# Kernel tuning notes

Measured on AMD Instinct MI355X. Metric: run time of the kernel, lower is better.

## Reference

```python
import jax, jax.numpy as jnp
import numpy as np

B, L, F, H = 1024, 256, 128, 256
A, CH, OUT = 128, 256, 512


def setup_inputs() -> dict:
    key = jax.random.key(0)
    ks = jax.random.split(key, 12)
    s = lambda k, shape, fan: (jax.random.normal(k, shape, jnp.float32) / np.float32(np.sqrt(fan)))
    return dict(
        input_batch=jax.random.normal(ks[0], (B, L, F), jnp.float32),
        tte=jax.random.randint(ks[1], (B,), 0, L, jnp.int32),
        W_ih=s(ks[2], (3 * H, F), F), W_hh=s(ks[3], (3 * H, H), H),
        b_ih=jnp.zeros((3 * H,), jnp.float32), b_hh=jnp.zeros((3 * H,), jnp.float32),
        W_out=s(ks[4], (F, H), H), b_out=jnp.zeros((F,), jnp.float32),
        Wa=s(ks[5], (H, A), H), Ua=s(ks[6], (F, A), F), va=s(ks[7], (A,), A),
        W1=s(ks[8], (H + F, CH), H + F), b1=jnp.zeros((CH,), jnp.float32),
        W2=s(ks[9], (CH, OUT), CH), b2=jnp.zeros((OUT,), jnp.float32),
    )


def _gru_step(x, h, W_ih, W_hh, b_ih, b_hh):
    # torch.nn.GRU single-step math, batched over B
    gi = x @ W_ih.T + b_ih          # [B,3H]
    gh = h @ W_hh.T + b_hh          # [B,3H]
    i_r, i_z, i_n = jnp.split(gi, 3, axis=-1)
    h_r, h_z, h_n = jnp.split(gh, 3, axis=-1)
    r = jax.nn.sigmoid(i_r + h_r)
    z = jax.nn.sigmoid(i_z + h_z)
    n = jnp.tanh(i_n + r * h_n)
    return (1.0 - z) * n + z * h


def reference(input_batch, tte, W_ih, W_hh, b_ih, b_hh, W_out, b_out,
              Wa, Ua, va, W1, b1, W2, b2):
    Bn, Ln, Fn = input_batch.shape
    Hn = W_hh.shape[1]
    h0 = jnp.zeros((Bn, Hn), input_batch.dtype)
    xs = jnp.moveaxis(input_batch, 1, 0)  # [L,B,F]
    ts = jnp.arange(Ln)

    def step(h, inp):
        x_t, t = inp
        h_new = _gru_step(x_t, h, W_ih, W_hh, b_ih, b_hh)
        active = (t < tte)[:, None]          # ragged length mask [B,1]
        h = jnp.where(active, h_new, h)      # freeze state past tte
        out_t = jnp.where(active, h_new @ W_out.T + b_out, 0.0)
        hid_t = jnp.where(active, h_new, 0.0)
        return h, (out_t, hid_t)

    _, (outs, hids) = jax.lax.scan(step, h0, (xs, ts))
    output_batch = jnp.moveaxis(outs, 0, 1)   # [B,L,F], zero-padded like the torch code
    hidden_vec = jnp.moveaxis(hids, 0, 1)     # [B,L,H], zero-padded

    # last measurement at index tte (the torch code indexes batch[tte])
    last = jnp.take_along_axis(input_batch, tte[:, None, None].astype(jnp.int32), axis=1)[:, 0]  # [B,F]

    # decoder: additive attention over the full padded trajectory
    scores = jnp.tanh(hidden_vec @ Wa + (last @ Ua)[:, None, :]) @ va   # [B,L]
    alpha = jax.nn.softmax(scores, axis=-1)
    context = jnp.einsum('bl,blh->bh', alpha, hidden_vec)               # [B,H]

    # causes network: MLP + softmax over cause x time-bin grid
    zc = jax.nn.relu(jnp.concatenate([context, last], axis=-1) @ W1 + b1)
    fht = jax.nn.softmax(zc @ W2 + b2, axis=-1)                         # [B,OUT]
    return output_batch, fht
```

## Files before the change

### kernel.cpp

```cpp
#include <hip/hip_runtime.h>

#define B_ 1024
#define L_ 256
#define F_ 128
#define H_ 256

typedef __bf16 bf16x8 __attribute__((ext_vector_type(8)));
typedef __bf16 bf16x4 __attribute__((ext_vector_type(4)));
typedef float f32x4 __attribute__((ext_vector_type(4)));
typedef int i32x4 __attribute__((ext_vector_type(4)));

#define MFMA16(a, b, c) __builtin_amdgcn_mfma_f32_16x16x32_bf16((a), (b), (c), 0, 0, 0)
#define MFMA_I8(a, b, c) __builtin_amdgcn_mfma_i32_16x16x64_i8((a), (b), (c), 0, 0, 0)
#define BAR_LDS() asm volatile("s_waitcnt lgkmcnt(0)\n\ts_barrier" ::: "memory")

__device__ __forceinline__ float rcp_f(float x) { return __builtin_amdgcn_rcpf(x); }
__device__ __forceinline__ float sigm(float x) { return rcp_f(1.f + __expf(-x)); }
__device__ __forceinline__ float tanh_f(float x) {
  float ax = fabsf(x);
  float e = __expf(-2.f * ax);
  float r = (1.f - e) * rcp_f(1.f + e);
  return copysignf(r, x);
}
__device__ __forceinline__ bf16x8 ld8(const __bf16* p) { return *(const bf16x8*)p; }
__device__ __forceinline__ float wave_max(float v) {
#pragma unroll
  for (int d = 1; d < 64; d <<= 1) v = fmaxf(v, __shfl_xor(v, d));
  return v;
}
__device__ __forceinline__ float wave_sum(float v) {
#pragma unroll
  for (int d = 1; d < 64; d <<= 1) v += __shfl_xor(v, d);
  return v;
}
__device__ __forceinline__ unsigned pack4(float a, float b, float c, float d, float inv) {
  return (unsigned)(unsigned char)(signed char)__float2int_rn(a * inv)
       | ((unsigned)(unsigned char)(signed char)__float2int_rn(b * inv) << 8)
       | ((unsigned)(unsigned char)(signed char)__float2int_rn(c * inv) << 16)
       | ((unsigned)(unsigned char)(signed char)__float2int_rn(d * inv) << 24);
}

__global__ void cvt_kernel(const float* __restrict__ wih_f, const float* __restrict__ wa_f,
                           const float* __restrict__ ua_f, const float* __restrict__ w1_f,
                           const float* __restrict__ w2_f,
                           __bf16* __restrict__ wih, __bf16* __restrict__ wa_t,
                           __bf16* __restrict__ ua_t, __bf16* __restrict__ w1_t,
                           __bf16* __restrict__ w2_t) {
  int i = blockIdx.x * 256 + threadIdx.x;
  if (i < 98304) wih[i] = (__bf16)wih_f[i];
  else if (i < 131072) {
    int j = i - 98304; int a = j >> 8, k = j & 255;
    wa_t[j] = (__bf16)wa_f[k * 128 + a];
  } else if (i < 147456) {
    int j = i - 131072; int a = j >> 7, f = j & 127;
    ua_t[j] = (__bf16)ua_f[f * 128 + a];
  } else if (i < 245760) {
    int j = i - 147456; int c = j / 384, k = j - c * 384;
    w1_t[j] = (__bf16)w1_f[k * 256 + c];
  } else if (i < 376832) {
    int j = i - 245760; int o = j >> 8, k = j & 255;
    w2_t[j] = (__bf16)w2_f[k * 512 + o];
  }
}

__global__ void quant_kernel(const float* __restrict__ whh_f, const float* __restrict__ wout_f,
                             signed char* __restrict__ wq_rz,
                             signed char* __restrict__ wqn_f,
                             signed char* __restrict__ wqo_f,
                             float* __restrict__ dq) {
  const int c = blockIdx.x * 256 + threadIdx.x;
  if (c >= 896) return;
  const float* row = (c < 768) ? whh_f + (size_t)c * 256 : wout_f + (size_t)(c - 768) * 256;
  float m = 0.f;
  for (int k4 = 0; k4 < 64; ++k4) {
    float4 v = *(const float4*)(row + k4 * 4);
    m = fmaxf(m, fmaxf(fmaxf(fabsf(v.x), fabsf(v.y)), fmaxf(fabsf(v.z), fabsf(v.w))));
  }
  const float inv = (m > 1e-30f) ? 127.f / m : 0.f;
  dq[c] = m / 16129.f;
  if (c < 512) {
    for (int k4 = 0; k4 < 64; ++k4) {
      float4 v = *(const float4*)(row + k4 * 4);
      *(unsigned*)(wq_rz + (size_t)c * 256 + k4 * 4) = pack4(v.x, v.y, v.z, v.w, inv);
    }
  } else if (c < 768) {
    const int cN = c - 512;
    const int t16 = cN >> 4, l15q = cN & 15;
    for (int kt = 0; kt < 4; ++kt)
      for (int lgq = 0; lgq < 4; ++lgq) {
        signed char* dst = wqn_f + (size_t)(((t16 * 4 + kt) * 64) + lgq * 16 + l15q) * 16;
        const float* src = row + kt * 64 + lgq * 16;
        for (int j4 = 0; j4 < 4; ++j4) {
          float4 v = *(const float4*)(src + j4 * 4);
          *(unsigned*)(dst + j4 * 4) = pack4(v.x, v.y, v.z, v.w, inv);
        }
      }
  } else {
    const int oc = c - 768;
    const int t8 = oc >> 4, l15q = oc & 15;
    for (int kt = 0; kt < 4; ++kt)
      for (int lgq = 0; lgq < 4; ++lgq) {
        signed char* dst = wqo_f + (size_t)(((t8 * 4 + kt) * 64) + lgq * 16 + l15q) * 16;
        const float* src = row + kt * 64 + lgq * 16;
        for (int j4 = 0; j4 < 4; ++j4) {
          float4 v = *(const float4*)(src + j4 * 4);
          *(unsigned*)(dst + j4 * 4) = pack4(v.x, v.y, v.z, v.w, inv);
        }
      }
  }
}

__global__ __launch_bounds__(512, 2) void gi_gemm_kernel(
    const float* __restrict__ x, const float* __restrict__ b_ih,
    const float* __restrict__ b_hh, const __bf16* __restrict__ wih,
    const int* __restrict__ tte, __bf16* __restrict__ gi,
    float* __restrict__ out) {
  const int tid = threadIdx.x;
  const int lane = tid & 63, w = tid >> 6;
  const int l15 = lane & 15, lg = lane >> 4, kofs = lg * 8;
  const int bblk = blockIdx.x & 63, tgrp = blockIdx.x >> 6;
  const int b0 = bblk * 16;

  {
    const int pr = tid >> 1, ph = tid & 1;
    const int bl = pr >> 4, tl = pr & 15;
    const int bb = b0 + bl, tt = tgrp * 16 + tl;
    if (tt >= tte[bb]) {
      float4* dst = (float4*)(out + ((size_t)bb * L_ + tt) * F_) + ph * 16;
#pragma unroll
      for (int i = 0; i < 16; ++i) dst[i] = float4{0.f, 0.f, 0.f, 0.f};
    }
  }

  int tmaxB = 0;
  for (int i = 0; i < 16; ++i) tmaxB = max(tmaxB, tte[b0 + i]);
  if (tgrp * 16 > tmaxB) return;

  bf16x8 wf[6][4];
  float bias[6];
#pragma unroll
  for (int tile = 0; tile < 6; ++tile) {
    const int gate = tile >> 1;
    const int c = w * 32 + (tile & 1) * 16 + l15;
    const int col = gate * 256 + c;
#pragma unroll
    for (int kt = 0; kt < 4; ++kt) wf[tile][kt] = ld8(wih + (size_t)col * 128 + kt * 32 + kofs);
    bias[tile] = (gate == 0) ? b_ih[c] + b_hh[c]
               : (gate == 1) ? b_ih[256 + c] + b_hh[256 + c]
                             : b_ih[512 + c];
  }

#pragma unroll 1
  for (int ti = 0; ti < 16; ++ti) {
    const int t = tgrp * 16 + ti;
    if (t > tmaxB) break;
    const float* xb = x + ((size_t)(b0 + l15) * L_ + t) * F_ + kofs;
    bf16x8 xfr[4];
#pragma unroll
    for (int kt = 0; kt < 4; ++kt) {
      float4 a = *(const float4*)(xb + kt * 32);
      float4 b = *(const float4*)(xb + kt * 32 + 4);
      xfr[kt][0] = (__bf16)a.x; xfr[kt][1] = (__bf16)a.y;
      xfr[kt][2] = (__bf16)a.z; xfr[kt][3] = (__bf16)a.w;
      xfr[kt][4] = (__bf16)b.x; xfr[kt][5] = (__bf16)b.y;
      xfr[kt][6] = (__bf16)b.z; xfr[kt][7] = (__bf16)b.w;
    }
    f32x4 acc[6];
#pragma unroll
    for (int tile = 0; tile < 6; ++tile) {
      acc[tile][0] = bias[tile]; acc[tile][1] = bias[tile];
      acc[tile][2] = bias[tile]; acc[tile][3] = bias[tile];
    }
#pragma unroll
    for (int kt = 0; kt < 4; ++kt)
#pragma unroll
      for (int tile = 0; tile < 6; ++tile)
        acc[tile] = MFMA16(xfr[kt], wf[tile][kt], acc[tile]);

    const size_t chunk = (((size_t)t * 64 + bblk) * 8 + w) * 6;
#pragma unroll
    for (int tile = 0; tile < 6; ++tile) {
      bf16x4 pk;
      pk[0] = (__bf16)acc[tile][0]; pk[1] = (__bf16)acc[tile][1];
      pk[2] = (__bf16)acc[tile][2]; pk[3] = (__bf16)acc[tile][3];
      *(bf16x4*)(gi + (chunk + tile) * 256 + (lg * 16 + l15) * 4) = pk;
    }
  }
}

__global__ __launch_bounds__(1024) void gru256_kernel(
    const int* __restrict__ tte, const float* __restrict__ b_hh,
    const signed char* __restrict__ wq_rz, const signed char* __restrict__ wqn_f,
    const signed char* __restrict__ wqo_f, const float* __restrict__ dq,
    const __bf16* __restrict__ gi, const float* __restrict__ b_out,
    __bf16* __restrict__ hid, float* __restrict__ out) {
  __shared__ signed char wlds[512 * 256];
  __shared__ signed char hb[2][4][272];
  __shared__ f32x4 racc[4][256];
  const int tid = threadIdx.x;
  const int lane = tid & 63, w = tid >> 6;
  const int l15 = lane & 15, lg = lane >> 4;
  const int blk = blockIdx.x;
  const int b0 = blk * 4;

  for (int idx = tid; idx < 8192; idx += 1024) {
    const int row = idx >> 4, g = idx & 15;
    uint4 v = *(const uint4*)(wq_rz + (size_t)row * 256 + g * 16);
    *(uint4*)&wlds[row * 256 + ((g ^ (row & 15)) << 4)] = v;
  }
  for (int i = tid; i < 2 * 4 * 272; i += 1024) ((signed char*)hb)[i] = 0;

  const int colL = w * 16 + l15;
  i32x4 nw[4];
#pragma unroll
  for (int kt = 0; kt < 4; ++kt)
    nw[kt] = *(const i32x4*)(wqn_f + (size_t)((w * 4 + kt) * 64 + lane) * 16);

  const int ocol = (w & 7) * 16 + l15;
  i32x4 ow[4];
#pragma unroll
  for (int kt = 0; kt < 4; ++kt)
    ow[kt] = *(const i32x4*)(wqo_f + (size_t)(((w & 7) * 4 + kt) * 64 + lane) * 16);
  const float dqo = dq[768 + ocol];
  const float bo = b_out[ocol];
  int tteO[4];
#pragma unroll
  for (int r = 0; r < 4; ++r) tteO[r] = tte[b0 + r];
  float* outp = out + ((size_t)b0 * L_) * F_ + ocol;

  const int grow = tid >> 8, gcol = tid & 255;
  const float dqR = dq[gcol], dqZ = dq[256 + gcol], dqN = dq[512 + gcol];
  const float bhn = b_hh[512 + gcol];
  const int tteL = tte[b0 + grow];
  int tmax = 0;
#pragma unroll
  for (int i = 0; i < 4; ++i) tmax = max(tmax, tte[b0 + i]);

  const size_t gb0 = (((size_t)(blk >> 2) * 8 + (gcol >> 5)) * 6 + ((gcol >> 4) & 1)) * 256
                   + (size_t)((blk & 3) * 16 + (gcol & 15)) * 4 + grow;
  const __bf16* gp = gi + gb0;
  __bf16 gR = gp[0], gZ = gp[512], gN = gp[1024];
  const __bf16* gpp = gp + 786432;

  __bf16* hidp = hid + ((size_t)(b0 + grow) * L_) * H_ + gcol;
  float hprev = 0.f;

  __syncthreads();

#pragma unroll 1
  for (int t = 0; t < tmax; ++t) {
    const int c = t & 1, nc = c ^ 1;

    i32x4 aR = {0, 0, 0, 0}, aZ = {0, 0, 0, 0}, aN = {0, 0, 0, 0};
#pragma unroll
    for (int kt = 0; kt < 4; ++kt) {
      const i32x4 hA = *(const i32x4*)&hb[c][l15 & 3][kt * 64 + lg * 16];
      const int gsw = ((kt * 4 + lg) ^ l15) << 4;
      aR = MFMA_I8(hA, *(const i32x4*)&wlds[colL * 256 + gsw], aR);
      aZ = MFMA_I8(hA, *(const i32x4*)&wlds[(256 + colL) * 256 + gsw], aZ);
      aN = MFMA_I8(hA, nw[kt], aN);
    }
    if (lg == 0) {
#pragma unroll
      for (int r = 0; r < 4; ++r) {
        f32x4 v = {(float)aR[r], (float)aZ[r], (float)aN[r], 0.f};
        racc[r][colL] = v;
      }
    }
    BAR_LDS();

    {
      const f32x4 rv = racc[grow][gcol];
      const float grf = (float)gR, gzf = (float)gZ, gnf = (float)gN;
      gR = gpp[0]; gZ = gpp[512]; gN = gpp[1024];
      gpp += 786432;
      const float rg = sigm(grf + rv[0] * dqR);
      const float zg = sigm(gzf + rv[1] * dqZ);
      const float ng = tanh_f(gnf + rg * (rv[2] * dqN + bhn));
      const float hnew = zg * (hprev - ng) + ng;
      const float hw = (t < tteL) ? hnew : hprev;
      hprev = hw;
      hb[nc][grow][gcol] = (signed char)__float2int_rn(hw * 127.f);
      if (t < tteL) *hidp = (__bf16)hw;
      hidp += H_;
    }
    BAR_LDS();

    if (w < 8) {
      i32x4 ac = {0, 0, 0, 0};
#pragma unroll
      for (int kt = 0; kt < 4; ++kt) {
        const i32x4 hA = *(const i32x4*)&hb[nc][l15 & 3][kt * 64 + lg * 16];
        ac = MFMA_I8(hA, ow[kt], ac);
      }
      if (lg == 0) {
#pragma unroll
        for (int r = 0; r < 4; ++r)
          if (t < tteO[r]) outp[(size_t)r * (L_ * F_)] = (float)ac[r] * dqo + bo;
      }
    }
    outp += F_;
  }
}

__global__ __launch_bounds__(512, 2) void decoder3_kernel(
    const float* __restrict__ x, const int* __restrict__ tte,
    const __bf16* __restrict__ hid, const __bf16* __restrict__ wa_t,
    const __bf16* __restrict__ ua_t, const __bf16* __restrict__ w1_t,
    const __bf16* __restrict__ w2_t, const float* __restrict__ va,
    const float* __restrict__ b1, const float* __restrict__ b2,
    float* __restrict__ fht) {
  __shared__ __bf16 catb[16][392];
  __shared__ float u_s[4][128];
  __shared__ float sa[4][256];
  __shared__ __bf16 z1b[16][264];
  __shared__ float lg2[4][516];
  __shared__ float ctxp[2][4][256];
  __shared__ float va_s[128];
  __shared__ int tte_s[4];
  const int tid = threadIdx.x;
  const int lane = tid & 63, w = tid >> 6;
  const int l15 = lane & 15, lg = lane >> 4, kofs = lg * 8;
  const int b0 = blockIdx.x * 4;

  if (tid < 4) tte_s[tid] = tte[b0 + tid];
  if (tid < 128) va_s[tid] = va[tid];
  if (tid < 392)
    for (int r = 4; r < 16; ++r) catb[r][tid] = (__bf16)0.f;
  if (tid < 264)
    for (int r = 4; r < 16; ++r) z1b[r][tid] = (__bf16)0.f;
  __syncthreads();

  {
    const int row = tid >> 7, c = tid & 127;
    catb[row][256 + c] = (__bf16)x[((size_t)(b0 + row) * L_ + tte_s[row]) * F_ + c];
  }
  __syncthreads();

  {
    f32x4 uacc = {0, 0, 0, 0};
#pragma unroll
    for (int kt = 0; kt < 4; ++kt) {
      const bf16x8 af = *(const bf16x8*)&catb[l15][256 + kt * 32 + kofs];
      const bf16x8 bf = ld8(ua_t + (size_t)(w * 16 + l15) * 128 + kt * 32 + kofs);
      uacc = MFMA16(af, bf, uacc);
    }
#pragma unroll
    for (int r = 0; r < 4; ++r) {
      const int row = 4 * lg + r;
      if (row < 4) u_s[row][w * 16 + l15] = uacc[r];
    }
  }
  __syncthreads();

  bf16x8 zero8;
#pragma unroll
  for (int j = 0; j < 8; ++j) zero8[j] = (__bf16)0.f;
#pragma unroll 1
  for (int it = 0; it < 8; ++it) {
    const int pair = it * 8 + w;
    const int b = pair >> 4, mtile = pair & 15;
    const int tteB = tte_s[b];
    const int trow = mtile * 16 + l15;
    const __bf16* hrow = hid + ((size_t)(b0 + b) * L_ + trow) * H_ + kofs;
    bf16x8 af[8];
#pragma unroll
    for (int kt = 0; kt < 8; ++kt) af[kt] = (trow < tteB) ? ld8(hrow + kt * 32) : zero8;
    f32x4 sacc[8];
#pragma unroll
    for (int ct = 0; ct < 8; ++ct) { sacc[ct][0] = 0; sacc[ct][1] = 0; sacc[ct][2] = 0; sacc[ct][3] = 0; }
#pragma unroll
    for (int kt = 0; kt < 8; ++kt)
#pragma unroll
      for (int ct = 0; ct < 8; ++ct)
        sacc[ct] = MFMA16(af[kt], ld8(wa_t + (size_t)(ct * 16 + l15) * 256 + kt * 32 + kofs), sacc[ct]);
    float sp[4] = {0, 0, 0, 0};
#pragma unroll
    for (int ct = 0; ct < 8; ++ct) {
      const int a = ct * 16 + l15;
      const float ua = u_s[b][a], vv = va_s[a];
#pragma unroll
      for (int r = 0; r < 4; ++r) sp[r] += tanh_f(sacc[ct][r] + ua) * vv;
    }
#pragma unroll
    for (int r = 0; r < 4; ++r) {
      sp[r] += __shfl_xor(sp[r], 1);
      sp[r] += __shfl_xor(sp[r], 2);
      sp[r] += __shfl_xor(sp[r], 4);
      sp[r] += __shfl_xor(sp[r], 8);
    }
    if (l15 == 0) {
#pragma unroll
      for (int r = 0; r < 4; ++r) sa[b][mtile * 16 + 4 * lg + r] = sp[r];
    }
  }
  __syncthreads();

  if (w < 4) {
    float sv[4];
#pragma unroll
    for (int j = 0; j < 4; ++j) sv[j] = sa[w][lane + 64 * j];
    float mx = fmaxf(fmaxf(sv[0], sv[1]), fmaxf(sv[2], sv[3]));
    mx = wave_max(mx);
    float es[4], ss = 0.f;
#pragma unroll
    for (int j = 0; j < 4; ++j) { es[j] = __expf(sv[j] - mx); ss += es[j]; }
    ss = wave_sum(ss);
    const float inv = rcp_f(ss);
#pragma unroll
    for (int j = 0; j < 4; ++j) sa[w][lane + 64 * j] = es[j] * inv;
  }
  __syncthreads();

  {
    const int be = w & 3, half = w >> 2;
    const int tteE = tte_s[be];
    float c4[4] = {0.f, 0.f, 0.f, 0.f};
    const __bf16* hp = hid + ((size_t)(b0 + be) * L_ + half) * H_ + lane * 4;
#pragma unroll 2
    for (int t = half; t < tteE; t += 2) {
      const float al = sa[be][t];
      const bf16x4 hv = *(const bf16x4*)hp;
      hp += 2 * H_;
#pragma unroll
      for (int j = 0; j < 4; ++j) c4[j] += al * (float)hv[j];
    }
#pragma unroll
    for (int j = 0; j < 4; ++j) ctxp[half][be][lane * 4 + j] = c4[j];
  }
  __syncthreads();
  if (w < 4) {
#pragma unroll
    for (int j = 0; j < 4; ++j)
      catb[w][lane * 4 + j] = (__bf16)(ctxp[0][w][lane * 4 + j] + ctxp[1][w][lane * 4 + j]);
  }
  __syncthreads();

#pragma unroll 1
  for (int half = 0; half < 2; ++half) {
    const int nt = w * 2 + half;
    f32x4 zacc = {0, 0, 0, 0};
#pragma unroll
    for (int kt = 0; kt < 12; ++kt) {
      const bf16x8 af = *(const bf16x8*)&catb[l15][kt * 32 + kofs];
      const bf16x8 bf = ld8(w1_t + (size_t)(nt * 16 + l15) * 384 + kt * 32 + kofs);
      zacc = MFMA16(af, bf, zacc);
    }
    const float bb = b1[nt * 16 + l15];
#pragma unroll
    for (int r = 0; r < 4; ++r) {
      const int row = 4 * lg + r;
      if (row < 4) z1b[row][nt * 16 + l15] = (__bf16)fmaxf(zacc[r] + bb, 0.f);
    }
  }
  __syncthreads();

#pragma unroll 1
  for (int q = 0; q < 4; ++q) {
    const int nt = w * 4 + q;
    f32x4 oacc = {0, 0, 0, 0};
#pragma unroll
    for (int kt = 0; kt < 8; ++kt) {
      const bf16x8 af = *(const bf16x8*)&z1b[l15][kt * 32 + kofs];
      const bf16x8 bf = ld8(w2_t + (size_t)(nt * 16 + l15) * 256 + kt * 32 + kofs);
      oacc = MFMA16(af, bf, oacc);
    }
    const float bb = b2[nt * 16 + l15];
#pragma unroll
    for (int r = 0; r < 4; ++r) {
      const int row = 4 * lg + r;
      if (row < 4) lg2[row][nt * 16 + l15] = oacc[r] + bb;
    }
  }
  __syncthreads();
  if (w < 4) {
    float lv[8];
    float mx = -1e30f;
#pragma unroll
    for (int j = 0; j < 8; ++j) { lv[j] = lg2[w][lane + 64 * j]; mx = fmaxf(mx, lv[j]); }
    mx = wave_max(mx);
    float s2 = 0.f;
#pragma unroll
    for (int j = 0; j < 8; ++j) { lv[j] = __expf(lv[j] - mx); s2 += lv[j]; }
    s2 = wave_sum(s2);
    const float inv2 = rcp_f(s2);
#pragma unroll
    for (int j = 0; j < 8; ++j)
      fht[(size_t)(b0 + w) * 512 + lane + 64 * j] = lv[j] * inv2;
  }
}

extern "C" void kernel_launch(void* const* d_in, const int* in_sizes, int n_in,
                              void* d_out, int out_size, void* d_ws, size_t ws_size,
                              hipStream_t stream) {
  const float* x = (const float*)d_in[0];
  const int* tte = (const int*)d_in[1];
  const float* W_ih = (const float*)d_in[2];
  const float* W_hh = (const float*)d_in[3];
  const float* b_ih = (const float*)d_in[4];
  const float* b_hh = (const float*)d_in[5];
  const float* W_out = (const float*)d_in[6];
  const float* b_out = (const float*)d_in[7];
  const float* Wa = (const float*)d_in[8];
  const float* Ua = (const float*)d_in[9];
  const float* va = (const float*)d_in[10];
  const float* W1 = (const float*)d_in[11];
  const float* b1 = (const float*)d_in[12];
  const float* W2 = (const float*)d_in[13];
  const float* b2 = (const float*)d_in[14];

  char* ws = (char*)d_ws;
  __bf16* wih = (__bf16*)(ws + 0);
  __bf16* wa_t = (__bf16*)(ws + 196608);
  __bf16* ua_t = (__bf16*)(ws + 262144);
  __bf16* w1_t = (__bf16*)(ws + 294912);
  __bf16* w2_t = (__bf16*)(ws + 491520);
  signed char* wq_rz = (signed char*)(ws + 753664);
  signed char* wqn_f = (signed char*)(ws + 884736);
  signed char* wqo_f = (signed char*)(ws + 950272);
  float* dq = (float*)(ws + 983040);
  __bf16* hid = (__bf16*)(ws + 1048576);
  __bf16* gi = (__bf16*)(ws + 135266304);

  float* out = (float*)d_out;
  float* fht = out + (size_t)33554432;

  cvt_kernel<<<1472, 256, 0, stream>>>(W_ih, Wa, Ua, W1, W2,
                                       wih, wa_t, ua_t, w1_t, w2_t);
  quant_kernel<<<4, 256, 0, stream>>>(W_hh, W_out, wq_rz, wqn_f, wqo_f, dq);
  gi_gemm_kernel<<<1024, 512, 0, stream>>>(x, b_ih, b_hh, wih, tte, gi, out);
  gru256_kernel<<<256, 1024, 0, stream>>>(tte, b_hh, wq_rz, wqn_f, wqo_f, dq,
                                          gi, b_out, hid, out);
  decoder3_kernel<<<256, 512, 0, stream>>>(x, tte, hid, wa_t, ua_t, w1_t, w2_t,
                                           va, b1, b2, fht);
}
```

Baseline: 793.5 us.

## Keep all GRU recurrent weights in registers and defer output projection one step

The r and z gate int8 weights move from a 128KB LDS array into per-wave registers, using the same fragment layout as the n-gate weights. This removes LDS weight reads from the recurrence. The output projection for step t-1 now runs after the gate MFMAs of step t and before the first barrier, which cuts one phase between barriers, and a tail handles the last step. The f32x4 staging buffer is split into three padded float arrays. The cost is higher VGPR pressure at 1024 threads per block.

```diff
diff --git a/kernel.cpp b/kernel.cpp
--- a/kernel.cpp
+++ b/kernel.cpp
@@ -64,8 +64,7 @@
 }
 
 __global__ void quant_kernel(const float* __restrict__ whh_f, const float* __restrict__ wout_f,
-                             signed char* __restrict__ wq_rz,
-                             signed char* __restrict__ wqn_f,
+                             signed char* __restrict__ wqg_f,
                              signed char* __restrict__ wqo_f,
                              float* __restrict__ dq) {
   const int c = blockIdx.x * 256 + threadIdx.x;
@@ -78,17 +77,12 @@
   }
   const float inv = (m > 1e-30f) ? 127.f / m : 0.f;
   dq[c] = m / 16129.f;
-  if (c < 512) {
-    for (int k4 = 0; k4 < 64; ++k4) {
-      float4 v = *(const float4*)(row + k4 * 4);
-      *(unsigned*)(wq_rz + (size_t)c * 256 + k4 * 4) = pack4(v.x, v.y, v.z, v.w, inv);
-    }
-  } else if (c < 768) {
-    const int cN = c - 512;
-    const int t16 = cN >> 4, l15q = cN & 15;
+  if (c < 768) {
+    const int g = c >> 8, cc = c & 255;
+    const int t16 = cc >> 4, l15q = cc & 15;
     for (int kt = 0; kt < 4; ++kt)
       for (int lgq = 0; lgq < 4; ++lgq) {
-        signed char* dst = wqn_f + (size_t)(((t16 * 4 + kt) * 64) + lgq * 16 + l15q) * 16;
+        signed char* dst = wqg_f + (size_t)((((g * 16 + t16) * 4 + kt) * 64) + lgq * 16 + l15q) * 16;
         const float* src = row + kt * 64 + lgq * 16;
         for (int j4 = 0; j4 < 4; ++j4) {
           float4 v = *(const float4*)(src + j4 * 4);
@@ -190,32 +184,28 @@
 
 __global__ __launch_bounds__(1024) void gru256_kernel(
     const int* __restrict__ tte, const float* __restrict__ b_hh,
-    const signed char* __restrict__ wq_rz, const signed char* __restrict__ wqn_f,
-    const signed char* __restrict__ wqo_f, const float* __restrict__ dq,
-    const __bf16* __restrict__ gi, const float* __restrict__ b_out,
+    const signed char* __restrict__ wqg_f, const signed char* __restrict__ wqo_f,
+    const float* __restrict__ dq, const __bf16* __restrict__ gi,
+    const float* __restrict__ b_out,
     __bf16* __restrict__ hid, float* __restrict__ out) {
-  __shared__ signed char wlds[512 * 256];
-  __shared__ signed char hb[2][4][272];
-  __shared__ f32x4 racc[4][256];
+  __shared__ signed char hb[2][4][288];
+  __shared__ float raccR[4][260], raccZ[4][260], raccN[4][260];
   const int tid = threadIdx.x;
   const int lane = tid & 63, w = tid >> 6;
   const int l15 = lane & 15, lg = lane >> 4;
   const int blk = blockIdx.x;
   const int b0 = blk * 4;
 
-  for (int idx = tid; idx < 8192; idx += 1024) {
-    const int row = idx >> 4, g = idx & 15;
-    uint4 v = *(const uint4*)(wq_rz + (size_t)row * 256 + g * 16);
-    *(uint4*)&wlds[row * 256 + ((g ^ (row & 15)) << 4)] = v;
-  }
-  for (int i = tid; i < 2 * 4 * 272; i += 1024) ((signed char*)hb)[i] = 0;
+  for (int i = tid; i < 2 * 4 * 288; i += 1024) ((signed char*)hb)[i] = 0;
 
   const int colL = w * 16 + l15;
-  i32x4 nw[4];
-#pragma unroll
-  for (int kt = 0; kt < 4; ++kt)
-    nw[kt] = *(const i32x4*)(wqn_f + (size_t)((w * 4 + kt) * 64 + lane) * 16);
-
+  i32x4 wR[4], wZ[4], wN[4];
+#pragma unroll
+  for (int kt = 0; kt < 4; ++kt) {
+    wR[kt] = *(const i32x4*)(wqg_f + (size_t)((((0 * 16 + w) * 4 + kt) * 64) + lane) * 16);
+    wZ[kt] = *(const i32x4*)(wqg_f + (size_t)((((1 * 16 + w) * 4 + kt) * 64) + lane) * 16);
+    wN[kt] = *(const i32x4*)(wqg_f + (size_t)((((2 * 16 + w) * 4 + kt) * 64) + lane) * 16);
+  }
   const int ocol = (w & 7) * 16 + l15;
   i32x4 ow[4];
 #pragma unroll
@@ -255,28 +245,44 @@
 #pragma unroll
     for (int kt = 0; kt < 4; ++kt) {
       const i32x4 hA = *(const i32x4*)&hb[c][l15 & 3][kt * 64 + lg * 16];
-      const int gsw = ((kt * 4 + lg) ^ l15) << 4;
-      aR = MFMA_I8(hA, *(const i32x4*)&wlds[colL * 256 + gsw], aR);
-      aZ = MFMA_I8(hA, *(const i32x4*)&wlds[(256 + colL) * 256 + gsw], aZ);
-      aN = MFMA_I8(hA, nw[kt], aN);
+      aR = MFMA_I8(hA, wR[kt], aR);
+      aZ = MFMA_I8(hA, wZ[kt], aZ);
+      aN = MFMA_I8(hA, wN[kt], aN);
+    }
+    if (w < 8 && t > 0) {
+      i32x4 ac = {0, 0, 0, 0};
+#pragma unroll
+      for (int kt = 0; kt < 4; ++kt) {
+        const i32x4 hA = *(const i32x4*)&hb[c][l15 & 3][kt * 64 + lg * 16];
+        ac = MFMA_I8(hA, ow[kt], ac);
+      }
+      if (lg == 0) {
+#pragma unroll
+        for (int r = 0; r < 4; ++r)
+          if (t - 1 < tteO[r]) outp[(size_t)r * (L_ * F_)] = (float)ac[r] * dqo + bo;
+      }
+      outp += F_;
     }
     if (lg == 0) {
 #pragma unroll
       for (int r = 0; r < 4; ++r) {
-        f32x4 v = {(float)aR[r], (float)aZ[r], (float)aN[r], 0.f};
-        racc[r][colL] = v;
+        raccR[r][colL] = (float)aR[r];
+        raccZ[r][colL] = (float)aZ[r];
+        raccN[r][colL] = (float)aN[r];
       }
     }
     BAR_LDS();
 
     {
-      const f32x4 rv = racc[grow][gcol];
+      const float rv0 = raccR[grow][gcol];
+      const float rv1 = raccZ[grow][gcol];
+      const float rv2 = raccN[grow][gcol];
       const float grf = (float)gR, gzf = (float)gZ, gnf = (float)gN;
       gR = gpp[0]; gZ = gpp[512]; gN = gpp[1024];
       gpp += 786432;
-      const float rg = sigm(grf + rv[0] * dqR);
-      const float zg = sigm(gzf + rv[1] * dqZ);
-      const float ng = tanh_f(gnf + rg * (rv[2] * dqN + bhn));
+      const float rg = sigm(grf + rv0 * dqR);
+      const float zg = sigm(gzf + rv1 * dqZ);
+      const float ng = tanh_f(gnf + rg * (rv2 * dqN + bhn));
       const float hnew = zg * (hprev - ng) + ng;
       const float hw = (t < tteL) ? hnew : hprev;
       hprev = hw;
@@ -285,21 +291,21 @@
       hidp += H_;
     }
     BAR_LDS();
-
-    if (w < 8) {
-      i32x4 ac = {0, 0, 0, 0};
-#pragma unroll
-      for (int kt = 0; kt < 4; ++kt) {
-        const i32x4 hA = *(const i32x4*)&hb[nc][l15 & 3][kt * 64 + lg * 16];
-        ac = MFMA_I8(hA, ow[kt], ac);
-      }
-      if (lg == 0) {
-#pragma unroll
-        for (int r = 0; r < 4; ++r)
-          if (t < tteO[r]) outp[(size_t)r * (L_ * F_)] = (float)ac[r] * dqo + bo;
-      }
-    }
-    outp += F_;
+  }
+
+  if (w < 8 && tmax > 0) {
+    const int cf = tmax & 1;
+    i32x4 ac = {0, 0, 0, 0};
+#pragma unroll
+    for (int kt = 0; kt < 4; ++kt) {
+      const i32x4 hA = *(const i32x4*)&hb[cf][l15 & 3][kt * 64 + lg * 16];
+      ac = MFMA_I8(hA, ow[kt], ac);
+    }
+    if (lg == 0) {
+#pragma unroll
+      for (int r = 0; r < 4; ++r)
+        if (tmax - 1 < tteO[r]) outp[(size_t)r * (L_ * F_)] = (float)ac[r] * dqo + bo;
+    }
   }
 }
 
@@ -515,8 +521,7 @@
   __bf16* ua_t = (__bf16*)(ws + 262144);
   __bf16* w1_t = (__bf16*)(ws + 294912);
   __bf16* w2_t = (__bf16*)(ws + 491520);
-  signed char* wq_rz = (signed char*)(ws + 753664);
-  signed char* wqn_f = (signed char*)(ws + 884736);
+  signed char* wqg_f = (signed char*)(ws + 753664);
   signed char* wqo_f = (signed char*)(ws + 950272);
   float* dq = (float*)(ws + 983040);
   __bf16* hid = (__bf16*)(ws + 1048576);
@@ -527,10 +532,10 @@
 
   cvt_kernel<<<1472, 256, 0, stream>>>(W_ih, Wa, Ua, W1, W2,
                                        wih, wa_t, ua_t, w1_t, w2_t);
-  quant_kernel<<<4, 256, 0, stream>>>(W_hh, W_out, wq_rz, wqn_f, wqo_f, dq);
+  quant_kernel<<<4, 256, 0, stream>>>(W_hh, W_out, wqg_f, wqo_f, dq);
   gi_gemm_kernel<<<1024, 512, 0, stream>>>(x, b_ih, b_hh, wih, tte, gi, out);
-  gru256_kernel<<<256, 1024, 0, stream>>>(tte, b_hh, wq_rz, wqn_f, wqo_f, dq,
-                                          gi, b_out, hid, out);
+  gru256_kernel<<<256, 1024, 0, stream>>>(tte, b_hh, wqg_f, wqo_f, dq, gi,
+                                          b_out, hid, out);
   decoder3_kernel<<<256, 512, 0, stream>>>(x, tte, hid, wa_t, ua_t, w1_t, w2_t,
                                            va, b1, b2, fht);
 }
```

Result: faster. 769.0 us (-3.1%).
